# Performance work log

Measured on AMD Instinct MI355X. Metric: run time of the kernel, lower is better.

Reference implementation:

```python
import jax, jax.numpy as jnp
import numpy as np

N, C = 65536, 512
DK = C // 2
B = 1024  # crystals; L = N // B atoms per crystal
BN_EPS = 1e-5
L1_EPS = 1e-9


def setup_inputs() -> dict:
    key = jax.random.key(0)
    ks = jax.random.split(key, 4)
    s = 1.0 / np.sqrt(C)
    return {
        "atom_fea": jax.random.normal(ks[0], (N, C), jnp.float32),
        # q_conv and k_conv share weight/bias in the original module -> single Wqk
        "Wqk": jax.random.normal(ks[1], (DK, C), jnp.float32) * s,
        "bqk": jnp.zeros((DK,), jnp.float32),
        "Wv": jax.random.normal(ks[2], (C, C), jnp.float32) * s,
        "bv": jnp.zeros((C,), jnp.float32),
        "Wt": jax.random.normal(ks[3], (C, C), jnp.float32) * s,
        "bt": jnp.zeros((C,), jnp.float32),
        "gamma": jnp.ones((C,), jnp.float32),
        "beta": jnp.zeros((C,), jnp.float32),
        "num_crystals": B,
    }


def reference(atom_fea, Wqk, bqk, Wv, bv, Wt, bt, gamma, beta, num_crystals):
    n, c = atom_fea.shape
    dk = Wqk.shape[0]
    b = num_crystals
    l = n // b  # atoms per crystal (equal-size segments)

    # 1x1 convs == linear projections; q and k are tied -> one projection
    qk = atom_fea @ Wqk.T + bqk          # [N, dk]
    v = atom_fea @ Wv.T + bv             # [N, C]

    qkb = qk.reshape(b, l, dk)
    vb = v.reshape(b, l, c)

    # per-crystal energy: [b, i(query), j(key)]
    energy = jnp.einsum("bid,bjd->bij", qkb, qkb) / jnp.sqrt(jnp.float32(dk))
    # softmax over dim=-2 (query axis), then L1-normalize over keys
    a = jax.nn.softmax(energy, axis=-2)
    att = a / (L1_EPS + a.sum(axis=-1, keepdims=True))

    x_r = jnp.einsum("bij,bjc->bic", att, vb).reshape(n, c)
    x_trans = atom_fea - x_r

    t = x_trans @ Wt.T + bt              # trans_conv (1x1)
    # BatchNorm1d in training mode: batch stats over the atom axis
    mean = t.mean(axis=0)
    var = t.var(axis=0)
    bn = (t - mean) * jax.lax.rsqrt(var + BN_EPS) * gamma + beta
    return atom_fea + jax.nn.relu(bn)
```

## Files before the change

### kernel.cpp

```cpp
#include <hip/hip_runtime.h>
#include <stdint.h>

#define NAT 65536
#define CH 512
#define NQKV 768

typedef __bf16 bf16x8 __attribute__((ext_vector_type(8)));
typedef float f32x4 __attribute__((ext_vector_type(4)));

union B8 { uint4 u; __bf16 h[8]; };

__device__ __forceinline__ void gload16(const void* g, void* l) {
  __builtin_amdgcn_global_load_lds((const __attribute__((address_space(1))) void*)g,
                                   (__attribute__((address_space(3))) void*)l, 16, 0, 0);
}

__global__ void k_prep(const float* __restrict__ atom, const float* __restrict__ wqk,
                       const float* __restrict__ bqk, const float* __restrict__ wv,
                       const float* __restrict__ bv, const float* __restrict__ wt,
                       __bf16* __restrict__ atom16, __bf16* __restrict__ wqkv16,
                       float* __restrict__ bqkv, __bf16* __restrict__ wt16,
                       float* __restrict__ stats)
{
  int tid = blockIdx.x * blockDim.x + threadIdx.x;
  int nth = gridDim.x * blockDim.x;
  const float4* a4 = (const float4*)atom;
  for (int i = tid; i < NAT * CH / 8; i += nth) {
    float4 x = a4[2 * i], y = a4[2 * i + 1];
    B8 u;
    u.h[0] = (__bf16)x.x; u.h[1] = (__bf16)x.y; u.h[2] = (__bf16)x.z; u.h[3] = (__bf16)x.w;
    u.h[4] = (__bf16)y.x; u.h[5] = (__bf16)y.y; u.h[6] = (__bf16)y.z; u.h[7] = (__bf16)y.w;
    ((uint4*)atom16)[i] = u.u;
  }
  for (int i = tid; i < NQKV * CH / 8; i += nth) {
    int row = (i * 8) >> 9;
    const float* src = (row < 256) ? (wqk + (size_t)i * 8) : (wv + (size_t)i * 8 - 256 * 512);
    float4 x = ((const float4*)src)[0], y = ((const float4*)src)[1];
    B8 u;
    u.h[0] = (__bf16)x.x; u.h[1] = (__bf16)x.y; u.h[2] = (__bf16)x.z; u.h[3] = (__bf16)x.w;
    u.h[4] = (__bf16)y.x; u.h[5] = (__bf16)y.y; u.h[6] = (__bf16)y.z; u.h[7] = (__bf16)y.w;
    ((uint4*)wqkv16)[i] = u.u;
  }
  for (int i = tid; i < CH * CH / 8; i += nth) {
    float4 x = ((const float4*)wt)[2 * i], y = ((const float4*)wt)[2 * i + 1];
    B8 u;
    u.h[0] = (__bf16)x.x; u.h[1] = (__bf16)x.y; u.h[2] = (__bf16)x.z; u.h[3] = (__bf16)x.w;
    u.h[4] = (__bf16)y.x; u.h[5] = (__bf16)y.y; u.h[6] = (__bf16)y.z; u.h[7] = (__bf16)y.w;
    ((uint4*)wt16)[i] = u.u;
  }
  if (tid < NQKV) bqkv[tid] = (tid < 256) ? bqk[tid] : bv[tid - 256];
  if (tid < 1024) stats[tid] = 0.f;
}

template<int NOUT, bool STATS>
__global__ __launch_bounds__(512, 4) void k_gemm(const __bf16* __restrict__ A,
    const __bf16* __restrict__ W, const float* __restrict__ bias,
    __bf16* __restrict__ Cout, float* __restrict__ stats)
{
  __shared__ __align__(16) char lds[49152];
  const int t = threadIdx.x, w = t >> 6, l = t & 63;
  const int wr = w >> 2, wc = w & 3;
  const int m0 = blockIdx.x * 128, n0 = blockIdx.y * 256;
  const int lrow = l >> 3;
  const int lslot = (l & 7) ^ lrow;
  f32x4 acc[4][4] = {};

  for (int kt = 0; kt < 8; ++kt) {
    const int k0 = kt * 64;
#pragma unroll
    for (int i = 0; i < 2; ++i) {
      int row = (i * 8 + w) * 8 + lrow;
      gload16(A + ((size_t)(m0 + row) * 512 + k0 + lslot * 8), lds + (i * 8 + w) * 1024);
    }
#pragma unroll
    for (int i = 0; i < 4; ++i) {
      int row = (i * 8 + w) * 8 + lrow;
      gload16(W + ((size_t)(n0 + row) * 512 + k0 + lslot * 8), lds + 16384 + (i * 8 + w) * 1024);
    }
    asm volatile("s_waitcnt vmcnt(0)" ::: "memory");
    __syncthreads();
#pragma unroll
    for (int ks = 0; ks < 2; ++ks) {
      bf16x8 af[4];
#pragma unroll
      for (int mi = 0; mi < 4; ++mi) {
        int r = wr * 64 + mi * 16 + (l & 15);
        af[mi] = *(const bf16x8*)(lds + r * 128 + (((ks * 4 + (l >> 4)) ^ (r & 7)) << 4));
      }
#pragma unroll
      for (int ni = 0; ni < 4; ++ni) {
        int r = wc * 64 + ni * 16 + (l & 15);
        bf16x8 bfr = *(const bf16x8*)(lds + 16384 + r * 128 + (((ks * 4 + (l >> 4)) ^ (r & 7)) << 4));
#pragma unroll
        for (int mi = 0; mi < 4; ++mi)
          acc[mi][ni] = __builtin_amdgcn_mfma_f32_16x16x32_bf16(af[mi], bfr, acc[mi][ni], 0, 0, 0);
      }
    }
    __syncthreads();
  }

  float ssum[4] = {0, 0, 0, 0}, ssq[4] = {0, 0, 0, 0};
#pragma unroll
  for (int ni = 0; ni < 4; ++ni) {
    int col = n0 + wc * 64 + ni * 16 + (l & 15);
    float bb = bias[col];
#pragma unroll
    for (int mi = 0; mi < 4; ++mi) {
#pragma unroll
      for (int r = 0; r < 4; ++r) {
        int row = m0 + wr * 64 + mi * 16 + (l >> 4) * 4 + r;
        float v = acc[mi][ni][r] + bb;
        Cout[(size_t)row * NOUT + col] = (__bf16)v;
        if (STATS) { ssum[ni] += v; ssq[ni] += v * v; }
      }
    }
  }
  if (STATS) {
#pragma unroll
    for (int ni = 0; ni < 4; ++ni) {
      float s = ssum[ni], q = ssq[ni];
      s += __shfl_xor(s, 16, 64); q += __shfl_xor(q, 16, 64);
      s += __shfl_xor(s, 32, 64); q += __shfl_xor(q, 32, 64);
      if (l < 16) {
        int col = n0 + wc * 64 + ni * 16 + l;
        atomicAdd(&stats[col], s);
        atomicAdd(&stats[512 + col], q);
      }
    }
  }
}

__global__ __launch_bounds__(256, 2) void k_attn(const __bf16* __restrict__ qkv,
    const __bf16* __restrict__ atom16, __bf16* __restrict__ xt)
{
  __shared__ __align__(16) char sm[49920];
  float* E = (float*)(sm + 32768);
  float* colinv = (float*)(sm + 49408);
  float* rowinv = (float*)(sm + 49664);
  const int t = threadIdx.x, w = t >> 6, l = t & 63;
  const size_t g0 = (size_t)blockIdx.x * 64;

#pragma unroll
  for (int i = 0; i < 8; ++i) {
    int chunk = i * 256 + t;
    int row = chunk >> 5, slot = chunk & 31;
    uint4 d = *(const uint4*)(qkv + (g0 + row) * NQKV + slot * 8);
    *(uint4*)(sm + row * 512 + ((slot ^ (row & 7)) << 4)) = d;
  }
  __syncthreads();

  f32x4 eacc[4] = {};
#pragma unroll
  for (int kk = 0; kk < 8; ++kk) {
    int ra = 16 * w + (l & 15);
    bf16x8 af = *(const bf16x8*)(sm + ra * 512 + (((kk * 4 + (l >> 4)) ^ (ra & 7)) << 4));
#pragma unroll
    for (int nj = 0; nj < 4; ++nj) {
      int rb = 16 * nj + (l & 15);
      bf16x8 bf_ = *(const bf16x8*)(sm + rb * 512 + (((kk * 4 + (l >> 4)) ^ (rb & 7)) << 4));
      eacc[nj] = __builtin_amdgcn_mfma_f32_16x16x32_bf16(af, bf_, eacc[nj], 0, 0, 0);
    }
  }
#pragma unroll
  for (int nj = 0; nj < 4; ++nj)
#pragma unroll
    for (int r = 0; r < 4; ++r) {
      int i = 16 * w + (l >> 4) * 4 + r;
      int j = 16 * nj + (l & 15);
      E[i * 65 + j] = eacc[nj][r] * 0.0625f;
    }
  __syncthreads();

  auto stage_v = [&](int h) {
#pragma unroll
    for (int ch = 0; ch < 8; ++ch) {
      int cb = w * 64 + ch * 8;
      B8 d; d.u = *(const uint4*)(qkv + (g0 + l) * NQKV + 256 + h * 256 + cb);
#pragma unroll
      for (int e = 0; e < 8; ++e) {
        int c = cb + e;
        *(__bf16*)(sm + c * 128 + (((l >> 3) ^ (c & 7)) << 4) + (l & 7) * 2) = d.h[e];
      }
    }
  };

  stage_v(0);

  {
    int j = t >> 2, sub = t & 3;
    float m = -1e30f;
#pragma unroll
    for (int k = 0; k < 16; ++k) m = fmaxf(m, E[(sub + 4 * k) * 65 + j]);
    m = fmaxf(m, __shfl_xor(m, 1)); m = fmaxf(m, __shfl_xor(m, 2));
    float s = 0.f;
#pragma unroll
    for (int k = 0; k < 16; ++k) {
      float e = __expf(E[(sub + 4 * k) * 65 + j] - m);
      E[(sub + 4 * k) * 65 + j] = e; s += e;
    }
    s += __shfl_xor(s, 1); s += __shfl_xor(s, 2);
    if (sub == 0) colinv[j] = 1.f / s;
  }
  __syncthreads();
  {
    int i = t >> 2, sub = t & 3;
    float rs = 0.f;
#pragma unroll
    for (int k = 0; k < 16; ++k) { int j = sub + 4 * k; rs += E[i * 65 + j] * colinv[j]; }
    rs += __shfl_xor(rs, 1); rs += __shfl_xor(rs, 2);
    if (sub == 0) rowinv[i] = 1.f / (1e-9f + rs);
  }
  __syncthreads();

  auto pv_out = [&](int h) {
    f32x4 acc[4][4] = {};
#pragma unroll
    for (int ks = 0; ks < 2; ++ks) {
      bf16x8 af[4];
#pragma unroll
      for (int mi = 0; mi < 4; ++mi) {
        int i = mi * 16 + (l & 15);
        float ri = rowinv[i];
        bf16x8 a;
#pragma unroll
        for (int e = 0; e < 8; ++e) {
          int j = ks * 32 + (l >> 4) * 8 + e;
          a[e] = (__bf16)(E[i * 65 + j] * colinv[j] * ri);
        }
        af[mi] = a;
      }
#pragma unroll
      for (int nc = 0; nc < 4; ++nc) {
        int c = w * 64 + nc * 16 + (l & 15);
        bf16x8 bfr = *(const bf16x8*)(sm + c * 128 + (((ks * 4 + (l >> 4)) ^ (c & 7)) << 4));
#pragma unroll
        for (int mi = 0; mi < 4; ++mi)
          acc[mi][nc] = __builtin_amdgcn_mfma_f32_16x16x32_bf16(af[mi], bfr, acc[mi][nc], 0, 0, 0);
      }
    }
    __syncthreads();
#pragma unroll
    for (int mi = 0; mi < 4; ++mi)
#pragma unroll
      for (int nc = 0; nc < 4; ++nc)
#pragma unroll
        for (int r = 0; r < 4; ++r) {
          int i = mi * 16 + (l >> 4) * 4 + r;
          int c = w * 64 + nc * 16 + (l & 15);
          int s = c >> 3;
          *(__bf16*)(sm + i * 512 + (((s ^ (i & 7))) << 4) + (c & 7) * 2) = (__bf16)acc[mi][nc][r];
        }
    __syncthreads();
#pragma unroll
    for (int j = 0; j < 8; ++j) {
      int chunk = j * 256 + t;
      int row = chunk >> 5, p = chunk & 31;
      int s = p ^ (row & 7);
      B8 xv; xv.u = *(const uint4*)(sm + row * 512 + p * 16);
      B8 av; av.u = *(const uint4*)(atom16 + (g0 + row) * 512 + h * 256 + s * 8);
      B8 o;
#pragma unroll
      for (int e = 0; e < 8; ++e) o.h[e] = (__bf16)((float)av.h[e] - (float)xv.h[e]);
      *(uint4*)(xt + (g0 + row) * 512 + h * 256 + s * 8) = o.u;
    }
  };

  pv_out(0);
  __syncthreads();
  stage_v(1);
  __syncthreads();
  pv_out(1);
}

__global__ void k_stats(const float* __restrict__ stats, const float* __restrict__ gamma,
                        const float* __restrict__ beta, float* __restrict__ ss)
{
  int c = threadIdx.x;
  float mean = stats[c] * (1.f / NAT);
  float var = stats[512 + c] * (1.f / NAT) - mean * mean;
  float sc = gamma[c] * rsqrtf(var + 1e-5f);
  ss[c] = sc;
  ss[512 + c] = beta[c] - mean * sc;
}

__global__ void k_final(const float* __restrict__ atom, const __bf16* __restrict__ tmat,
                        const float* __restrict__ ss, float* __restrict__ out)
{
  int tid = blockIdx.x * blockDim.x + threadIdx.x;
  int nth = gridDim.x * blockDim.x;
  for (int i = tid; i < NAT * CH / 8; i += nth) {
    int colb = (i & 63) * 8;
    B8 tv; tv.u = ((const uint4*)tmat)[i];
    float4 a0 = ((const float4*)atom)[2 * i], a1 = ((const float4*)atom)[2 * i + 1];
    float4 s0 = *(const float4*)(ss + colb), s1 = *(const float4*)(ss + colb + 4);
    float4 h0 = *(const float4*)(ss + 512 + colb), h1 = *(const float4*)(ss + 512 + colb + 4);
    float4 o0, o1;
    o0.x = a0.x + fmaxf(0.f, (float)tv.h[0] * s0.x + h0.x);
    o0.y = a0.y + fmaxf(0.f, (float)tv.h[1] * s0.y + h0.y);
    o0.z = a0.z + fmaxf(0.f, (float)tv.h[2] * s0.z + h0.z);
    o0.w = a0.w + fmaxf(0.f, (float)tv.h[3] * s0.w + h0.w);
    o1.x = a1.x + fmaxf(0.f, (float)tv.h[4] * s1.x + h1.x);
    o1.y = a1.y + fmaxf(0.f, (float)tv.h[5] * s1.y + h1.y);
    o1.z = a1.z + fmaxf(0.f, (float)tv.h[6] * s1.z + h1.z);
    o1.w = a1.w + fmaxf(0.f, (float)tv.h[7] * s1.w + h1.w);
    ((float4*)out)[2 * i] = o0;
    ((float4*)out)[2 * i + 1] = o1;
  }
}

extern "C" void kernel_launch(void* const* d_in, const int* in_sizes, int n_in,
                              void* d_out, int out_size, void* d_ws, size_t ws_size,
                              hipStream_t stream) {
  const float* atom  = (const float*)d_in[0];
  const float* wqk   = (const float*)d_in[1];
  const float* bqk   = (const float*)d_in[2];
  const float* wv    = (const float*)d_in[3];
  const float* bv    = (const float*)d_in[4];
  const float* wt    = (const float*)d_in[5];
  const float* bt    = (const float*)d_in[6];
  const float* gamma = (const float*)d_in[7];
  const float* beta  = (const float*)d_in[8];
  char* ws = (char*)d_ws;

  __bf16* atom16 = (__bf16*)(ws);
  __bf16* xtr    = (__bf16*)(ws);
  __bf16* qkv    = (__bf16*)(ws + 67108864);
  __bf16* tmat   = (__bf16*)(ws + 67108864);
  __bf16* wqkv16 = (__bf16*)(ws + 167772160);
  __bf16* wt16   = (__bf16*)(ws + 168558592);
  float*  bqkv   = (float*)(ws + 169082880);
  float*  stats  = (float*)(ws + 169085952);
  float*  ss     = (float*)(ws + 169090048);
  float*  out    = (float*)d_out;

  k_prep<<<dim3(2048), dim3(256), 0, stream>>>(atom, wqk, bqk, wv, bv, wt,
                                               atom16, wqkv16, bqkv, wt16, stats);
  k_gemm<NQKV, false><<<dim3(512, 3), dim3(512), 0, stream>>>(atom16, wqkv16, bqkv, qkv, nullptr);
  k_attn<<<dim3(1024), dim3(256), 0, stream>>>(qkv, atom16, xtr);
  k_gemm<CH, true><<<dim3(512, 2), dim3(512), 0, stream>>>(xtr, wt16, bt, tmat, stats);
  k_stats<<<dim3(1), dim3(512), 0, stream>>>(stats, gamma, beta, ss);
  k_final<<<dim3(2048), dim3(256), 0, stream>>>(atom, tmat, ss, out);
}
```

Before: 476.0 us.

## Overlap next K-tile global loads with MFMA in GEMM, fold BN stats into final

The GEMM main loop now reads both k-substeps of fragments from LDS into registers, syncs, then issues the async global-to-LDS loads for the next K tile before running the MFMAs at raised priority. This hides load latency behind compute within a single LDS buffer. The launch bound's min-blocks hint is dropped, which changes register limits and occupancy. The separate k_stats kernel is removed and the final kernel computes scale and shift per element, saving a launch but adding per-element rsqrt and stat loads.

```diff
diff --git a/kernel.cpp b/kernel.cpp
--- a/kernel.cpp
+++ b/kernel.cpp
@@ -53,7 +53,7 @@
 }
 
 template<int NOUT, bool STATS>
-__global__ __launch_bounds__(512, 4) void k_gemm(const __bf16* __restrict__ A,
+__global__ __launch_bounds__(512) void k_gemm(const __bf16* __restrict__ A,
     const __bf16* __restrict__ W, const float* __restrict__ bias,
     __bf16* __restrict__ Cout, float* __restrict__ stats)
 {
@@ -65,7 +65,7 @@
   const int lslot = (l & 7) ^ lrow;
   f32x4 acc[4][4] = {};
 
-  for (int kt = 0; kt < 8; ++kt) {
+  auto stage = [&](int kt) {
     const int k0 = kt * 64;
 #pragma unroll
     for (int i = 0; i < 2; ++i) {
@@ -77,26 +77,43 @@
       int row = (i * 8 + w) * 8 + lrow;
       gload16(W + ((size_t)(n0 + row) * 512 + k0 + lslot * 8), lds + 16384 + (i * 8 + w) * 1024);
     }
-    asm volatile("s_waitcnt vmcnt(0)" ::: "memory");
-    __syncthreads();
+  };
+
+  stage(0);
+  asm volatile("s_waitcnt vmcnt(0)" ::: "memory");
+  __builtin_amdgcn_s_barrier();
+
+  for (int kt = 0; kt < 8; ++kt) {
+    bf16x8 af[2][4], bfr[2][4];
 #pragma unroll
     for (int ks = 0; ks < 2; ++ks) {
-      bf16x8 af[4];
 #pragma unroll
       for (int mi = 0; mi < 4; ++mi) {
         int r = wr * 64 + mi * 16 + (l & 15);
-        af[mi] = *(const bf16x8*)(lds + r * 128 + (((ks * 4 + (l >> 4)) ^ (r & 7)) << 4));
+        af[ks][mi] = *(const bf16x8*)(lds + r * 128 + (((ks * 4 + (l >> 4)) ^ (r & 7)) << 4));
       }
 #pragma unroll
       for (int ni = 0; ni < 4; ++ni) {
         int r = wc * 64 + ni * 16 + (l & 15);
-        bf16x8 bfr = *(const bf16x8*)(lds + 16384 + r * 128 + (((ks * 4 + (l >> 4)) ^ (r & 7)) << 4));
+        bfr[ks][ni] = *(const bf16x8*)(lds + 16384 + r * 128 + (((ks * 4 + (l >> 4)) ^ (r & 7)) << 4));
+      }
+    }
+    asm volatile("s_waitcnt lgkmcnt(0)" ::: "memory");
+    __builtin_amdgcn_s_barrier();
+    if (kt < 7) stage(kt + 1);
+    __builtin_amdgcn_s_setprio(1);
+#pragma unroll
+    for (int ks = 0; ks < 2; ++ks)
+#pragma unroll
+      for (int ni = 0; ni < 4; ++ni)
 #pragma unroll
         for (int mi = 0; mi < 4; ++mi)
-          acc[mi][ni] = __builtin_amdgcn_mfma_f32_16x16x32_bf16(af[mi], bfr, acc[mi][ni], 0, 0, 0);
-      }
-    }
-    __syncthreads();
+          acc[mi][ni] = __builtin_amdgcn_mfma_f32_16x16x32_bf16(af[ks][mi], bfr[ks][ni], acc[mi][ni], 0, 0, 0);
+    __builtin_amdgcn_s_setprio(0);
+    if (kt < 7) {
+      asm volatile("s_waitcnt vmcnt(0)" ::: "memory");
+      __builtin_amdgcn_s_barrier();
+    }
   }
 
   float ssum[4] = {0, 0, 0, 0}, ssq[4] = {0, 0, 0, 0};
@@ -272,37 +289,29 @@
   pv_out(1);
 }
 
-__global__ void k_stats(const float* __restrict__ stats, const float* __restrict__ gamma,
-                        const float* __restrict__ beta, float* __restrict__ ss)
-{
-  int c = threadIdx.x;
-  float mean = stats[c] * (1.f / NAT);
-  float var = stats[512 + c] * (1.f / NAT) - mean * mean;
-  float sc = gamma[c] * rsqrtf(var + 1e-5f);
-  ss[c] = sc;
-  ss[512 + c] = beta[c] - mean * sc;
-}
-
 __global__ void k_final(const float* __restrict__ atom, const __bf16* __restrict__ tmat,
-                        const float* __restrict__ ss, float* __restrict__ out)
+                        const float* __restrict__ stats, const float* __restrict__ gamma,
+                        const float* __restrict__ beta, float* __restrict__ out)
 {
   int tid = blockIdx.x * blockDim.x + threadIdx.x;
   int nth = gridDim.x * blockDim.x;
+  const float invn = 1.f / NAT;
   for (int i = tid; i < NAT * CH / 8; i += nth) {
     int colb = (i & 63) * 8;
     B8 tv; tv.u = ((const uint4*)tmat)[i];
     float4 a0 = ((const float4*)atom)[2 * i], a1 = ((const float4*)atom)[2 * i + 1];
-    float4 s0 = *(const float4*)(ss + colb), s1 = *(const float4*)(ss + colb + 4);
-    float4 h0 = *(const float4*)(ss + 512 + colb), h1 = *(const float4*)(ss + 512 + colb + 4);
     float4 o0, o1;
-    o0.x = a0.x + fmaxf(0.f, (float)tv.h[0] * s0.x + h0.x);
-    o0.y = a0.y + fmaxf(0.f, (float)tv.h[1] * s0.y + h0.y);
-    o0.z = a0.z + fmaxf(0.f, (float)tv.h[2] * s0.z + h0.z);
-    o0.w = a0.w + fmaxf(0.f, (float)tv.h[3] * s0.w + h0.w);
-    o1.x = a1.x + fmaxf(0.f, (float)tv.h[4] * s1.x + h1.x);
-    o1.y = a1.y + fmaxf(0.f, (float)tv.h[5] * s1.y + h1.y);
-    o1.z = a1.z + fmaxf(0.f, (float)tv.h[6] * s1.z + h1.z);
-    o1.w = a1.w + fmaxf(0.f, (float)tv.h[7] * s1.w + h1.w);
+#pragma unroll
+    for (int e = 0; e < 8; ++e) {
+      int c = colb + e;
+      float mean = stats[c] * invn;
+      float var = stats[512 + c] * invn - mean * mean;
+      float sc = gamma[c] * rsqrtf(var + 1e-5f);
+      float sh = beta[c] - mean * sc;
+      float av = (e < 4) ? ((const float*)&a0)[e] : ((const float*)&a1)[e - 4];
+      float v = av + fmaxf(0.f, (float)tv.h[e] * sc + sh);
+      if (e < 4) ((float*)&o0)[e] = v; else ((float*)&o1)[e - 4] = v;
+    }
     ((float4*)out)[2 * i] = o0;
     ((float4*)out)[2 * i + 1] = o1;
   }
@@ -330,7 +339,6 @@
   __bf16* wt16   = (__bf16*)(ws + 168558592);
   float*  bqkv   = (float*)(ws + 169082880);
   float*  stats  = (float*)(ws + 169085952);
-  float*  ss     = (float*)(ws + 169090048);
   float*  out    = (float*)d_out;
 
   k_prep<<<dim3(2048), dim3(256), 0, stream>>>(atom, wqk, bqk, wv, bv, wt,
@@ -338,6 +346,5 @@
   k_gemm<NQKV, false><<<dim3(512, 3), dim3(512), 0, stream>>>(atom16, wqkv16, bqkv, qkv, nullptr);
   k_attn<<<dim3(1024), dim3(256), 0, stream>>>(qkv, atom16, xtr);
   k_gemm<CH, true><<<dim3(512, 2), dim3(512), 0, stream>>>(xtr, wt16, bt, tmat, stats);
-  k_stats<<<dim3(1), dim3(512), 0, stream>>>(stats, gamma, beta, ss);
-  k_final<<<dim3(2048), dim3(256), 0, stream>>>(atom, tmat, ss, out);
-}
+  k_final<<<dim3(2048), dim3(256), 0, stream>>>(atom, tmat, stats, gamma, beta, out);
+}
```

Measured after the change: 504.2 us. 5.9% more time.
